# Optimization experiments

Measured on AMD Instinct MI355X. Metric: run time of the kernel, lower is better.

## Reference

```python
import jax, jax.numpy as jnp
import numpy as np

ATOM_FEA = 128
NBR_FEA = 64
NUM_NBR = 12
N_NODES = 50000
N_EDGES = N_NODES * NUM_NBR
BN_EPS = 1e-5


def setup_inputs() -> dict:
    key = jax.random.key(0)
    ks = jax.random.split(key, 8)
    x = jax.random.normal(ks[0], (N_NODES, ATOM_FEA), dtype=jnp.float32)
    # CGCNN layout: each node has exactly NUM_NBR edges, contiguous by source node
    src = jnp.repeat(jnp.arange(N_NODES, dtype=jnp.int64), NUM_NBR)
    nbr = jax.random.randint(ks[1], (N_EDGES,), 0, N_NODES, dtype=jnp.int64)
    edge_index = jnp.stack([src, nbr], axis=0)
    edge_attr = jax.random.normal(ks[2], (N_EDGES, NBR_FEA), dtype=jnp.float32)
    in_dim = 2 * ATOM_FEA + NBR_FEA
    out_dim = 2 * ATOM_FEA
    lim = 1.0 / np.sqrt(in_dim)
    W = jax.random.uniform(ks[3], (out_dim, in_dim), jnp.float32, -lim, lim)
    b = jax.random.uniform(ks[4], (out_dim,), jnp.float32, -lim, lim)
    bn1_g = jnp.ones((out_dim,), jnp.float32)
    bn1_b = jnp.zeros((out_dim,), jnp.float32)
    bn2_g = jnp.ones((ATOM_FEA,), jnp.float32)
    bn2_b = jnp.zeros((ATOM_FEA,), jnp.float32)
    return {"x": x, "edge_index": edge_index, "edge_attr": edge_attr,
            "W": W, "b": b, "bn1_g": bn1_g, "bn1_b": bn1_b,
            "bn2_g": bn2_g, "bn2_b": bn2_b}


def _batchnorm(h, gamma, beta):
    # training-mode BN: biased batch variance, eps=1e-5 (torch default)
    mean = jnp.mean(h, axis=0)
    var = jnp.var(h, axis=0)
    return (h - mean) * jax.lax.rsqrt(var + BN_EPS) * gamma + beta


def reference(x, edge_index, edge_attr, W, b, bn1_g, bn1_b, bn2_g, bn2_b):
    n_nodes, fea = x.shape
    num_nbr = edge_index.shape[1] // n_nodes
    # gather + concat: [E, 2F + nbr_fea]
    total = jnp.concatenate([x[edge_index[1]], x[edge_index[0]], edge_attr], axis=1)
    gated = total @ W.T + b                      # [E, 2F]
    gated = _batchnorm(gated, bn1_g, bn1_b)
    nbr_filter, nbr_core = jnp.split(gated, 2, axis=1)
    msg = jax.nn.sigmoid(nbr_filter) * jax.nn.softplus(nbr_core)  # [E, F]
    nbr_sumed = msg.reshape(n_nodes, num_nbr, fea).sum(axis=1)    # [N, F]
    nbr_sumed = _batchnorm(nbr_sumed, bn2_g, bn2_b)
    return jax.nn.softplus(x + nbr_sumed)
```

## Files before the change

kernel.cpp:

```cpp
#include <hip/hip_runtime.h>
#include <math.h>

#define ATOM_FEA 128
#define NBR_FEA  64
#define IN_DIM   320
#define OUT_DIM  256

#define M_TILE   48
#define GRID_G   1024

typedef float  f32x4 __attribute__((ext_vector_type(4)));
typedef short  s16x8 __attribute__((ext_vector_type(8)));

__device__ __forceinline__ float softplusf(float v) {
    float e = __expf(-fabsf(v));
    return fmaxf(v, 0.f) + __logf(1.f + e);
}
__device__ __forceinline__ float sigmoidf(float v) {
    return __builtin_amdgcn_rcpf(1.f + __expf(-v));
}
__device__ __forceinline__ unsigned short f2bf(float f) {
    unsigned u = __float_as_uint(f);
    return (unsigned short)((u + 0x7FFFu + ((u >> 16) & 1u)) >> 16);
}
__device__ __forceinline__ float bf2f(unsigned short h) {
    return __uint_as_float(((unsigned)h) << 16);
}
__device__ __forceinline__ unsigned pk2(float a, float b) {
    return (unsigned)f2bf(a) | ((unsigned)f2bf(b) << 16);
}

#define EA_OFF   0
#define EA_STR   144
#define X_OFF    6912
#define X_STR    520
#define SMEM2    31872

__global__ __launch_bounds__(256) void k1_nodegemm(
    const float* __restrict__ x, const float* __restrict__ W,
    float* __restrict__ A, float* __restrict__ B, int nNodes)
{
    __shared__ float sx[64][68];
    __shared__ float sw[64][68];
    const int tx = threadIdx.x & 15;
    const int ty = threadIdx.x >> 4;
    const int cTile = blockIdx.x * 64;
    const int nTile = blockIdx.y * 64;
    const int rBase = (cTile < 256) ? cTile : (cTile - 256);
    const int kBase = (cTile < 256) ? 0 : 128;

    float acc[4][4] = {};
    for (int kc = 0; kc < 2; ++kc) {
        int idx = threadIdx.x;
        #pragma unroll
        for (int i = 0; i < 4; ++i, idx += 256) {
            int n = idx >> 4, q = idx & 15;
            float4 v = make_float4(0.f, 0.f, 0.f, 0.f);
            int gn = nTile + n;
            if (gn < nNodes)
                v = *(const float4*)(x + (size_t)gn * ATOM_FEA + kc * 64 + q * 4);
            *(float4*)(&sx[n][q * 4]) = v;
        }
        idx = threadIdx.x;
        #pragma unroll
        for (int i = 0; i < 4; ++i, idx += 256) {
            int c = idx >> 4, q = idx & 15;
            float4 v = *(const float4*)(W + (size_t)(rBase + c) * IN_DIM + kBase + kc * 64 + q * 4);
            sw[q * 4 + 0][c] = v.x; sw[q * 4 + 1][c] = v.y;
            sw[q * 4 + 2][c] = v.z; sw[q * 4 + 3][c] = v.w;
        }
        __syncthreads();
        #pragma unroll
        for (int k = 0; k < 64; k += 2) {
            float4 w0 = *(const float4*)(&sw[k][tx * 4]);
            float4 w1 = *(const float4*)(&sw[k + 1][tx * 4]);
            float2 xv[4];
            #pragma unroll
            for (int i = 0; i < 4; ++i)
                xv[i] = *(const float2*)(&sx[ty * 4 + i][k]);
            #pragma unroll
            for (int i = 0; i < 4; ++i) {
                acc[i][0] = fmaf(xv[i].x, w0.x, fmaf(xv[i].y, w1.x, acc[i][0]));
                acc[i][1] = fmaf(xv[i].x, w0.y, fmaf(xv[i].y, w1.y, acc[i][1]));
                acc[i][2] = fmaf(xv[i].x, w0.z, fmaf(xv[i].y, w1.z, acc[i][2]));
                acc[i][3] = fmaf(xv[i].x, w0.w, fmaf(xv[i].y, w1.w, acc[i][3]));
            }
        }
        __syncthreads();
    }
    float* dst = (cTile < 256) ? A : B;
    const int cOff = (cTile < 256) ? cTile : (cTile - 256);
    #pragma unroll
    for (int i = 0; i < 4; ++i) {
        int gn = nTile + ty * 4 + i;
        if (gn < nNodes) {
            float4 v = make_float4(acc[i][0], acc[i][1], acc[i][2], acc[i][3]);
            *(float4*)(dst + (size_t)gn * 256 + cOff + tx * 4) = v;
        }
    }
}

__global__ __launch_bounds__(256) void k2_fused(
    const float* __restrict__ A, const float* __restrict__ Bm,
    const float* __restrict__ ea, const int* __restrict__ ei,
    const float* __restrict__ W, const float* __restrict__ bvec,
    unsigned short* __restrict__ gated, float* __restrict__ part,
    int nNodes, int nEdges)
{
    __shared__ alignas(16) char smem[SMEM2];
    const int tid  = threadIdx.x;
    const int wave = tid >> 6;
    const int lane = tid & 63;
    const int li   = lane & 15;
    const int quad = lane >> 4;

    s16x8 bfr[2][4];
    #pragma unroll
    for (int ks = 0; ks < 2; ++ks)
        #pragma unroll
        for (int ns = 0; ns < 4; ++ns) {
            int chn = wave * 64 + ns * 16 + li;
            const float* wr = W + (size_t)chn * IN_DIM + 256 + ks * 32 + quad * 8;
            float4 va = *(const float4*)wr;
            float4 vb = *(const float4*)(wr + 4);
            union { uint4 u; s16x8 v; } cv;
            cv.u = make_uint4(pk2(va.x, va.y), pk2(va.z, va.w),
                              pk2(vb.x, vb.y), pk2(vb.z, vb.w));
            bfr[ks][ns] = cv.v;
        }

    const int chq = lane;
    const float4 b4 = *(const float4*)(bvec + chq * 4);
    float4 s4  = {0.f, 0.f, 0.f, 0.f};
    float4 s24 = {0.f, 0.f, 0.f, 0.f};

    const int nTiles = (nEdges + M_TILE - 1) / M_TILE;
    for (int t = blockIdx.x; t < nTiles; t += gridDim.x) {
        const int tBase = t * M_TILE;
        #pragma unroll
        for (int i = 0; i < 3; ++i) {
            int idx = tid + i * 256;
            int r = idx >> 4, q = idx & 15;
            int ge = tBase + r;
            float4 v = make_float4(0.f, 0.f, 0.f, 0.f);
            if (ge < nEdges) v = *(const float4*)(ea + (size_t)ge * 64 + q * 4);
            uint2 u; u.x = pk2(v.x, v.y); u.y = pk2(v.z, v.w);
            *(uint2*)(smem + EA_OFF + r * EA_STR + q * 8) = u;
        }
        __syncthreads();

        s16x8 af[2][3];
        #pragma unroll
        for (int ks = 0; ks < 2; ++ks)
            #pragma unroll
            for (int ms = 0; ms < 3; ++ms)
                af[ks][ms] = *(const s16x8*)(smem + EA_OFF + (ms * 16 + li) * EA_STR + (ks * 32 + quad * 8) * 2);

        f32x4 acc[3][4] = {};
        #pragma unroll
        for (int ks = 0; ks < 2; ++ks)
            #pragma unroll
            for (int ms = 0; ms < 3; ++ms)
                #pragma unroll
                for (int ns = 0; ns < 4; ++ns)
                    acc[ms][ns] = __builtin_amdgcn_mfma_f32_16x16x32_bf16(
                        af[ks][ms], bfr[ks][ns], acc[ms][ns], 0, 0, 0);

        #pragma unroll
        for (int ms = 0; ms < 3; ++ms)
            #pragma unroll
            for (int ns = 0; ns < 4; ++ns) {
                int col = wave * 64 + ns * 16 + li;
                #pragma unroll
                for (int r = 0; r < 4; ++r) {
                    int row = ms * 16 + quad * 4 + r;
                    *(unsigned short*)(smem + X_OFF + row * X_STR + col * 2) = f2bf(acc[ms][ns][r]);
                }
            }
        __syncthreads();

        const int node = t * 4 + wave;
        if (node < nNodes) {
            const float4 Bn = *(const float4*)(Bm + (size_t)node * 256 + chq * 4);
            const int e0 = tBase + wave * 12;
            #pragma unroll
            for (int j = 0; j < 12; ++j) {
                const int e = e0 + j;
                const int nb = ei[nEdges + e];
                float4 a4 = *(const float4*)(A + (size_t)nb * 256 + chq * 4);
                uint2 xv = *(const uint2*)(smem + X_OFF + (wave * 12 + j) * X_STR + chq * 8);
                float g0 = bf2f((unsigned short)(xv.x & 0xffffu)) + a4.x + Bn.x + b4.x;
                float g1 = bf2f((unsigned short)(xv.x >> 16))     + a4.y + Bn.y + b4.y;
                float g2 = bf2f((unsigned short)(xv.y & 0xffffu)) + a4.z + Bn.z + b4.z;
                float g3 = bf2f((unsigned short)(xv.y >> 16))     + a4.w + Bn.w + b4.w;
                s4.x += g0; s4.y += g1; s4.z += g2; s4.w += g3;
                s24.x = fmaf(g0, g0, s24.x); s24.y = fmaf(g1, g1, s24.y);
                s24.z = fmaf(g2, g2, s24.z); s24.w = fmaf(g3, g3, s24.w);
                uint2 o; o.x = pk2(g0, g1); o.y = pk2(g2, g3);
                *(uint2*)(gated + (size_t)e * 256 + chq * 4) = o;
            }
        }
    }

    __syncthreads();
    float* red = (float*)smem;
    *(float4*)(red + (size_t)(wave * 64 + chq) * 8)     = s4;
    *(float4*)(red + (size_t)(wave * 64 + chq) * 8 + 4) = s24;
    __syncthreads();
    {
        const int c = tid;
        const int g = c >> 2, k = c & 3;
        float s = 0.f, s2 = 0.f;
        #pragma unroll
        for (int w = 0; w < 4; ++w) {
            s  += red[(w * 64 + g) * 8 + k];
            s2 += red[(w * 64 + g) * 8 + 4 + k];
        }
        part[(size_t)blockIdx.x * 512 + c]       = s;
        part[(size_t)blockIdx.x * 512 + 256 + c] = s2;
    }
}

__global__ __launch_bounds__(1024) void k2b_reduce(
    const float* __restrict__ part, const float* __restrict__ g1v,
    const float* __restrict__ b1v, float* __restrict__ stats,
    int nBlocks, float invE)
{
    __shared__ float4 red[8][128];
    const int cq = threadIdx.x & 127;
    const int g  = threadIdx.x >> 7;
    float4 s = {0.f, 0.f, 0.f, 0.f};
    for (int i = g; i < nBlocks; i += 8) {
        float4 v = *(const float4*)(part + (size_t)i * 512 + cq * 4);
        s.x += v.x; s.y += v.y; s.z += v.z; s.w += v.w;
    }
    red[g][cq] = s;
    __syncthreads();
    if (threadIdx.x < 256) {
        const int c = threadIdx.x;
        float sT = 0.f, s2T = 0.f;
        #pragma unroll
        for (int w = 0; w < 8; ++w) {
            const float* r = (const float*)&red[w][0];
            sT  += r[c];
            s2T += r[256 + c];
        }
        float mean = sT * invE;
        float var = fmaf(-mean, mean, s2T * invE);
        float sc = g1v[c] * rsqrtf(var + 1e-5f);
        stats[c] = sc;
        stats[256 + c] = fmaf(-mean, sc, b1v[c]);
    }
}

__global__ __launch_bounds__(256) void k3_msg2(
    const unsigned short* __restrict__ gated, const float* __restrict__ stats,
    float* __restrict__ NS, float* __restrict__ part2, int nNodes)
{
    const int tid = threadIdx.x;
    const int o  = tid & 15;
    const int nl = tid >> 4;
    float scF[8], shF[8], scC[8], shC[8];
    #pragma unroll
    for (int k = 0; k < 8; ++k) {
        int cf = o * 8 + k;
        scF[k] = stats[cf];        shF[k] = stats[256 + cf];
        scC[k] = stats[128 + cf];  shC[k] = stats[384 + cf];
    }
    float sA[8] = {}, s2A[8] = {};
    for (int n = blockIdx.x * 16 + nl; n < nNodes; n += gridDim.x * 16) {
        float m[8] = {};
        for (int j = 0; j < 12; ++j) {
            size_t base = (size_t)(n * 12 + j) * 256;
            uint4 uf = *(const uint4*)(gated + base + o * 8);
            uint4 uc = *(const uint4*)(gated + base + 128 + o * 8);
            unsigned fu[4] = {uf.x, uf.y, uf.z, uf.w};
            unsigned cu[4] = {uc.x, uc.y, uc.z, uc.w};
            #pragma unroll
            for (int q = 0; q < 4; ++q) {
                float f0 = fmaf(bf2f((unsigned short)(fu[q] & 0xffffu)), scF[q*2],   shF[q*2]);
                float f1 = fmaf(bf2f((unsigned short)(fu[q] >> 16)),     scF[q*2+1], shF[q*2+1]);
                float c0 = fmaf(bf2f((unsigned short)(cu[q] & 0xffffu)), scC[q*2],   shC[q*2]);
                float c1 = fmaf(bf2f((unsigned short)(cu[q] >> 16)),     scC[q*2+1], shC[q*2+1]);
                m[q*2]   = fmaf(sigmoidf(f0), softplusf(c0), m[q*2]);
                m[q*2+1] = fmaf(sigmoidf(f1), softplusf(c1), m[q*2+1]);
            }
        }
        float4 o0 = {m[0], m[1], m[2], m[3]};
        float4 o1 = {m[4], m[5], m[6], m[7]};
        *(float4*)(NS + (size_t)n * 128 + o * 8)     = o0;
        *(float4*)(NS + (size_t)n * 128 + o * 8 + 4) = o1;
        #pragma unroll
        for (int k = 0; k < 8; ++k) {
            sA[k] += m[k];
            s2A[k] = fmaf(m[k], m[k], s2A[k]);
        }
    }
    __shared__ float red[2][16][128];
    #pragma unroll
    for (int k = 0; k < 8; ++k) {
        red[0][nl][o * 8 + k] = sA[k];
        red[1][nl][o * 8 + k] = s2A[k];
    }
    __syncthreads();
    if (tid < 128) {
        float s = 0.f, s2 = 0.f;
        #pragma unroll
        for (int r = 0; r < 16; ++r) {
            s  += red[0][r][tid];
            s2 += red[1][r][tid];
        }
        part2[(size_t)blockIdx.x * 256 + tid]       = s;
        part2[(size_t)blockIdx.x * 256 + 128 + tid] = s2;
    }
}

__global__ __launch_bounds__(1024) void k3b_reduce(
    const float* __restrict__ part2, const float* __restrict__ g2v,
    const float* __restrict__ b2v, float* __restrict__ stats2,
    int nBlocks, float invN)
{
    __shared__ float4 red[16][64];
    const int cq = threadIdx.x & 63;
    const int g  = threadIdx.x >> 6;
    float4 s = {0.f, 0.f, 0.f, 0.f};
    for (int i = g; i < nBlocks; i += 16) {
        float4 v = *(const float4*)(part2 + (size_t)i * 256 + cq * 4);
        s.x += v.x; s.y += v.y; s.z += v.z; s.w += v.w;
    }
    red[g][cq] = s;
    __syncthreads();
    if (threadIdx.x < 128) {
        const int c = threadIdx.x;
        float sT = 0.f, s2T = 0.f;
        #pragma unroll
        for (int w = 0; w < 16; ++w) {
            const float* r = (const float*)&red[w][0];
            sT  += r[c];
            s2T += r[128 + c];
        }
        float mean = sT * invN;
        float var = fmaf(-mean, mean, s2T * invN);
        float sc = g2v[c] * rsqrtf(var + 1e-5f);
        stats2[c] = sc;
        stats2[128 + c] = fmaf(-mean, sc, b2v[c]);
    }
}

__global__ __launch_bounds__(256) void k4_final(
    const float* __restrict__ x, const float* __restrict__ ns,
    const float* __restrict__ stats2, float* __restrict__ out, int total4)
{
    int idx = blockIdx.x * 256 + threadIdx.x;
    for (int i = idx; i < total4; i += gridDim.x * 256) {
        int cq = i & 31;
        float4 xv = ((const float4*)x)[i];
        float4 sv = ((const float4*)ns)[i];
        float4 sc = ((const float4*)stats2)[cq];
        float4 sh = ((const float4*)(stats2 + 128))[cq];
        float4 o;
        o.x = softplusf(fmaf(sv.x, sc.x, sh.x) + xv.x);
        o.y = softplusf(fmaf(sv.y, sc.y, sh.y) + xv.y);
        o.z = softplusf(fmaf(sv.z, sc.z, sh.z) + xv.z);
        o.w = softplusf(fmaf(sv.w, sc.w, sh.w) + xv.w);
        ((float4*)out)[i] = o;
    }
}

extern "C" void kernel_launch(void* const* d_in, const int* in_sizes, int n_in,
                              void* d_out, int out_size, void* d_ws, size_t ws_size,
                              hipStream_t stream)
{
    const float* x   = (const float*)d_in[0];
    const int*   ei  = (const int*)d_in[1];
    const float* ea  = (const float*)d_in[2];
    const float* W   = (const float*)d_in[3];
    const float* b   = (const float*)d_in[4];
    const float* g1v = (const float*)d_in[5];
    const float* b1v = (const float*)d_in[6];
    const float* g2v = (const float*)d_in[7];
    const float* b2v = (const float*)d_in[8];
    float* out = (float*)d_out;

    const int nNodes = in_sizes[0] / ATOM_FEA;
    const int nEdges = in_sizes[1] / 2;

    float* ws = (float*)d_ws;
    float* A   = ws;
    float* Bm  = A   + (size_t)nNodes * 256;
    float* NS  = Bm  + (size_t)nNodes * 256;
    float* P1  = NS  + (size_t)nNodes * 128;
    float* P2  = P1  + (size_t)GRID_G * 512;
    float* S1  = P2  + (size_t)GRID_G * 256;
    float* S2  = S1  + 512;
    unsigned short* gated = (unsigned short*)(S2 + 256);
    (void)ws_size; (void)n_in; (void)out_size;

    dim3 grid1(8, (nNodes + 63) / 64);
    k1_nodegemm<<<grid1, 256, 0, stream>>>(x, W, A, Bm, nNodes);

    k2_fused<<<GRID_G, 256, 0, stream>>>(A, Bm, ea, ei, W, b, gated, P1, nNodes, nEdges);
    k2b_reduce<<<1, 1024, 0, stream>>>(P1, g1v, b1v, S1, GRID_G, 1.f / (float)nEdges);
    k3_msg2<<<GRID_G, 256, 0, stream>>>(gated, S1, NS, P2, nNodes);
    k3b_reduce<<<1, 1024, 0, stream>>>(P2, g2v, b2v, S2, GRID_G, 1.f / (float)nNodes);
    k4_final<<<2048, 256, 0, stream>>>(x, NS, S2, out, nNodes * 32);
}
```

Before: 675.3 us.

## Use MFMA bf16 node GEMM, bf16 A/B tables, two-stage stat reductions

```diff
diff --git a/kernel.cpp b/kernel.cpp
--- a/kernel.cpp
+++ b/kernel.cpp
@@ -7,7 +7,9 @@
 #define OUT_DIM  256
 
 #define M_TILE   48
-#define GRID_G   1024
+#define GRID_G   768
+#define GRID_3   1024
+#define RB1      32
 
 typedef float  f32x4 __attribute__((ext_vector_type(4)));
 typedef short  s16x8 __attribute__((ext_vector_type(8)));
@@ -36,72 +38,73 @@
 #define X_STR    520
 #define SMEM2    31872
 
-__global__ __launch_bounds__(256) void k1_nodegemm(
+__global__ __launch_bounds__(256) void k1_mfma(
     const float* __restrict__ x, const float* __restrict__ W,
-    float* __restrict__ A, float* __restrict__ B, int nNodes)
-{
-    __shared__ float sx[64][68];
-    __shared__ float sw[64][68];
-    const int tx = threadIdx.x & 15;
-    const int ty = threadIdx.x >> 4;
+    unsigned short* __restrict__ Abf, unsigned short* __restrict__ Bbf,
+    int nNodes)
+{
+    __shared__ alignas(16) char sx[64 * 272];
+    const int tid  = threadIdx.x;
+    const int wave = tid >> 6;
+    const int lane = tid & 63;
+    const int li   = lane & 15;
+    const int quad = lane >> 4;
     const int cTile = blockIdx.x * 64;
     const int nTile = blockIdx.y * 64;
-    const int rBase = (cTile < 256) ? cTile : (cTile - 256);
+    const int cOff  = (cTile < 256) ? cTile : (cTile - 256);
     const int kBase = (cTile < 256) ? 0 : 128;
-
-    float acc[4][4] = {};
-    for (int kc = 0; kc < 2; ++kc) {
-        int idx = threadIdx.x;
-        #pragma unroll
-        for (int i = 0; i < 4; ++i, idx += 256) {
-            int n = idx >> 4, q = idx & 15;
-            float4 v = make_float4(0.f, 0.f, 0.f, 0.f);
-            int gn = nTile + n;
-            if (gn < nNodes)
-                v = *(const float4*)(x + (size_t)gn * ATOM_FEA + kc * 64 + q * 4);
-            *(float4*)(&sx[n][q * 4]) = v;
-        }
-        idx = threadIdx.x;
-        #pragma unroll
-        for (int i = 0; i < 4; ++i, idx += 256) {
-            int c = idx >> 4, q = idx & 15;
-            float4 v = *(const float4*)(W + (size_t)(rBase + c) * IN_DIM + kBase + kc * 64 + q * 4);
-            sw[q * 4 + 0][c] = v.x; sw[q * 4 + 1][c] = v.y;
-            sw[q * 4 + 2][c] = v.z; sw[q * 4 + 3][c] = v.w;
-        }
-        __syncthreads();
-        #pragma unroll
-        for (int k = 0; k < 64; k += 2) {
-            float4 w0 = *(const float4*)(&sw[k][tx * 4]);
-            float4 w1 = *(const float4*)(&sw[k + 1][tx * 4]);
-            float2 xv[4];
-            #pragma unroll
-            for (int i = 0; i < 4; ++i)
-                xv[i] = *(const float2*)(&sx[ty * 4 + i][k]);
-            #pragma unroll
-            for (int i = 0; i < 4; ++i) {
-                acc[i][0] = fmaf(xv[i].x, w0.x, fmaf(xv[i].y, w1.x, acc[i][0]));
-                acc[i][1] = fmaf(xv[i].x, w0.y, fmaf(xv[i].y, w1.y, acc[i][1]));
-                acc[i][2] = fmaf(xv[i].x, w0.z, fmaf(xv[i].y, w1.z, acc[i][2]));
-                acc[i][3] = fmaf(xv[i].x, w0.w, fmaf(xv[i].y, w1.w, acc[i][3]));
-            }
-        }
-        __syncthreads();
-    }
-    float* dst = (cTile < 256) ? A : B;
-    const int cOff = (cTile < 256) ? cTile : (cTile - 256);
-    #pragma unroll
-    for (int i = 0; i < 4; ++i) {
-        int gn = nTile + ty * 4 + i;
-        if (gn < nNodes) {
-            float4 v = make_float4(acc[i][0], acc[i][1], acc[i][2], acc[i][3]);
-            *(float4*)(dst + (size_t)gn * 256 + cOff + tx * 4) = v;
-        }
-    }
+    unsigned short* dst = (cTile < 256) ? Abf : Bbf;
+
+    s16x8 bf[4][4];
+    #pragma unroll
+    for (int ks = 0; ks < 4; ++ks)
+        #pragma unroll
+        for (int ns = 0; ns < 4; ++ns) {
+            const float* wr = W + (size_t)(cOff + ns * 16 + li) * IN_DIM + kBase + ks * 32 + quad * 8;
+            float4 va = *(const float4*)wr;
+            float4 vb = *(const float4*)(wr + 4);
+            union { uint4 u; s16x8 v; } cv;
+            cv.u = make_uint4(pk2(va.x, va.y), pk2(va.z, va.w),
+                              pk2(vb.x, vb.y), pk2(vb.z, vb.w));
+            bf[ks][ns] = cv.v;
+        }
+
+    #pragma unroll
+    for (int i = 0; i < 8; ++i) {
+        int idx = tid + i * 256;
+        int r = idx >> 5, q = idx & 31;
+        int gn = nTile + r;
+        float4 v = make_float4(0.f, 0.f, 0.f, 0.f);
+        if (gn < nNodes) v = *(const float4*)(x + (size_t)gn * ATOM_FEA + q * 4);
+        uint2 u; u.x = pk2(v.x, v.y); u.y = pk2(v.z, v.w);
+        *(uint2*)(sx + r * 272 + q * 8) = u;
+    }
+    __syncthreads();
+
+    s16x8 af[4];
+    #pragma unroll
+    for (int ks = 0; ks < 4; ++ks)
+        af[ks] = *(const s16x8*)(sx + (wave * 16 + li) * 272 + (ks * 32 + quad * 8) * 2);
+
+    f32x4 acc[4] = {};
+    #pragma unroll
+    for (int ks = 0; ks < 4; ++ks)
+        #pragma unroll
+        for (int ns = 0; ns < 4; ++ns)
+            acc[ns] = __builtin_amdgcn_mfma_f32_16x16x32_bf16(af[ks], bf[ks][ns], acc[ns], 0, 0, 0);
+
+    #pragma unroll
+    for (int ns = 0; ns < 4; ++ns)
+        #pragma unroll
+        for (int r = 0; r < 4; ++r) {
+            int node = nTile + wave * 16 + quad * 4 + r;
+            if (node < nNodes)
+                dst[(size_t)node * 256 + cOff + ns * 16 + li] = f2bf(acc[ns][r]);
+        }
 }
 
 __global__ __launch_bounds__(256) void k2_fused(
-    const float* __restrict__ A, const float* __restrict__ Bm,
+    const unsigned short* __restrict__ Abf, const unsigned short* __restrict__ Bbf,
     const float* __restrict__ ea, const int* __restrict__ ei,
     const float* __restrict__ W, const float* __restrict__ bvec,
     unsigned short* __restrict__ gated, float* __restrict__ part,
@@ -181,18 +184,22 @@
 
         const int node = t * 4 + wave;
         if (node < nNodes) {
-            const float4 Bn = *(const float4*)(Bm + (size_t)node * 256 + chq * 4);
+            uint2 bn2 = *(const uint2*)(Bbf + (size_t)node * 256 + chq * 4);
+            const float Bn0 = bf2f((unsigned short)(bn2.x & 0xffffu));
+            const float Bn1 = bf2f((unsigned short)(bn2.x >> 16));
+            const float Bn2 = bf2f((unsigned short)(bn2.y & 0xffffu));
+            const float Bn3 = bf2f((unsigned short)(bn2.y >> 16));
             const int e0 = tBase + wave * 12;
             #pragma unroll
             for (int j = 0; j < 12; ++j) {
                 const int e = e0 + j;
                 const int nb = ei[nEdges + e];
-                float4 a4 = *(const float4*)(A + (size_t)nb * 256 + chq * 4);
+                uint2 a2 = *(const uint2*)(Abf + (size_t)nb * 256 + chq * 4);
                 uint2 xv = *(const uint2*)(smem + X_OFF + (wave * 12 + j) * X_STR + chq * 8);
-                float g0 = bf2f((unsigned short)(xv.x & 0xffffu)) + a4.x + Bn.x + b4.x;
-                float g1 = bf2f((unsigned short)(xv.x >> 16))     + a4.y + Bn.y + b4.y;
-                float g2 = bf2f((unsigned short)(xv.y & 0xffffu)) + a4.z + Bn.z + b4.z;
-                float g3 = bf2f((unsigned short)(xv.y >> 16))     + a4.w + Bn.w + b4.w;
+                float g0 = bf2f((unsigned short)(xv.x & 0xffffu)) + bf2f((unsigned short)(a2.x & 0xffffu)) + Bn0 + b4.x;
+                float g1 = bf2f((unsigned short)(xv.x >> 16))     + bf2f((unsigned short)(a2.x >> 16))     + Bn1 + b4.y;
+                float g2 = bf2f((unsigned short)(xv.y & 0xffffu)) + bf2f((unsigned short)(a2.y & 0xffffu)) + Bn2 + b4.z;
+                float g3 = bf2f((unsigned short)(xv.y >> 16))     + bf2f((unsigned short)(a2.y >> 16))     + Bn3 + b4.w;
                 s4.x += g0; s4.y += g1; s4.z += g2; s4.w += g3;
                 s24.x = fmaf(g0, g0, s24.x); s24.y = fmaf(g1, g1, s24.y);
                 s24.z = fmaf(g2, g2, s24.z); s24.w = fmaf(g3, g3, s24.w);
@@ -221,36 +228,31 @@
     }
 }
 
-__global__ __launch_bounds__(1024) void k2b_reduce(
-    const float* __restrict__ part, const float* __restrict__ g1v,
-    const float* __restrict__ b1v, float* __restrict__ stats,
-    int nBlocks, float invE)
-{
-    __shared__ float4 red[8][128];
-    const int cq = threadIdx.x & 127;
-    const int g  = threadIdx.x >> 7;
-    float4 s = {0.f, 0.f, 0.f, 0.f};
-    for (int i = g; i < nBlocks; i += 8) {
-        float4 v = *(const float4*)(part + (size_t)i * 512 + cq * 4);
-        s.x += v.x; s.y += v.y; s.z += v.z; s.w += v.w;
-    }
-    red[g][cq] = s;
-    __syncthreads();
-    if (threadIdx.x < 256) {
-        const int c = threadIdx.x;
-        float sT = 0.f, s2T = 0.f;
-        #pragma unroll
-        for (int w = 0; w < 8; ++w) {
-            const float* r = (const float*)&red[w][0];
-            sT  += r[c];
-            s2T += r[256 + c];
-        }
-        float mean = sT * invE;
-        float var = fmaf(-mean, mean, s2T * invE);
-        float sc = g1v[c] * rsqrtf(var + 1e-5f);
-        stats[c] = sc;
-        stats[256 + c] = fmaf(-mean, sc, b1v[c]);
-    }
+__global__ __launch_bounds__(512) void k2b1(
+    const float* __restrict__ part, float* __restrict__ out, int nRows, int rowsPerBlk)
+{
+    const int c = threadIdx.x;
+    int r0 = blockIdx.x * rowsPerBlk;
+    int r1 = min(r0 + rowsPerBlk, nRows);
+    float s = 0.f;
+    for (int r = r0; r < r1; ++r) s += part[(size_t)r * 512 + c];
+    out[(size_t)blockIdx.x * 512 + c] = s;
+}
+__global__ __launch_bounds__(256) void k2b2(
+    const float* __restrict__ p1, const float* __restrict__ g1v,
+    const float* __restrict__ b1v, float* __restrict__ stats, float invE)
+{
+    const int c = threadIdx.x;
+    float s = 0.f, s2 = 0.f;
+    for (int r = 0; r < RB1; ++r) {
+        s  += p1[(size_t)r * 512 + c];
+        s2 += p1[(size_t)r * 512 + 256 + c];
+    }
+    float mean = s * invE;
+    float var = fmaf(-mean, mean, s2 * invE);
+    float sc = g1v[c] * rsqrtf(var + 1e-5f);
+    stats[c] = sc;
+    stats[256 + c] = fmaf(-mean, sc, b1v[c]);
 }
 
 __global__ __launch_bounds__(256) void k3_msg2(
@@ -315,36 +317,31 @@
     }
 }
 
-__global__ __launch_bounds__(1024) void k3b_reduce(
-    const float* __restrict__ part2, const float* __restrict__ g2v,
-    const float* __restrict__ b2v, float* __restrict__ stats2,
-    int nBlocks, float invN)
-{
-    __shared__ float4 red[16][64];
-    const int cq = threadIdx.x & 63;
-    const int g  = threadIdx.x >> 6;
-    float4 s = {0.f, 0.f, 0.f, 0.f};
-    for (int i = g; i < nBlocks; i += 16) {
-        float4 v = *(const float4*)(part2 + (size_t)i * 256 + cq * 4);
-        s.x += v.x; s.y += v.y; s.z += v.z; s.w += v.w;
-    }
-    red[g][cq] = s;
-    __syncthreads();
-    if (threadIdx.x < 128) {
-        const int c = threadIdx.x;
-        float sT = 0.f, s2T = 0.f;
-        #pragma unroll
-        for (int w = 0; w < 16; ++w) {
-            const float* r = (const float*)&red[w][0];
-            sT  += r[c];
-            s2T += r[128 + c];
-        }
-        float mean = sT * invN;
-        float var = fmaf(-mean, mean, s2T * invN);
-        float sc = g2v[c] * rsqrtf(var + 1e-5f);
-        stats2[c] = sc;
-        stats2[128 + c] = fmaf(-mean, sc, b2v[c]);
-    }
+__global__ __launch_bounds__(256) void k3b1(
+    const float* __restrict__ part2, float* __restrict__ out, int nRows, int rowsPerBlk)
+{
+    const int c = threadIdx.x;
+    int r0 = blockIdx.x * rowsPerBlk;
+    int r1 = min(r0 + rowsPerBlk, nRows);
+    float s = 0.f;
+    for (int r = r0; r < r1; ++r) s += part2[(size_t)r * 256 + c];
+    out[(size_t)blockIdx.x * 256 + c] = s;
+}
+__global__ __launch_bounds__(128) void k3b2(
+    const float* __restrict__ p1, const float* __restrict__ g2v,
+    const float* __restrict__ b2v, float* __restrict__ stats2, float invN)
+{
+    const int c = threadIdx.x;
+    float s = 0.f, s2 = 0.f;
+    for (int r = 0; r < RB1; ++r) {
+        s  += p1[(size_t)r * 256 + c];
+        s2 += p1[(size_t)r * 256 + 128 + c];
+    }
+    float mean = s * invN;
+    float var = fmaf(-mean, mean, s2 * invN);
+    float sc = g2v[c] * rsqrtf(var + 1e-5f);
+    stats2[c] = sc;
+    stats2[128 + c] = fmaf(-mean, sc, b2v[c]);
 }
 
 __global__ __launch_bounds__(256) void k4_final(
@@ -385,23 +382,26 @@
     const int nNodes = in_sizes[0] / ATOM_FEA;
     const int nEdges = in_sizes[1] / 2;
 
-    float* ws = (float*)d_ws;
-    float* A   = ws;
-    float* Bm  = A   + (size_t)nNodes * 256;
-    float* NS  = Bm  + (size_t)nNodes * 256;
+    unsigned short* Abf   = (unsigned short*)d_ws;
+    unsigned short* Bbf   = Abf + (size_t)nNodes * 256;
+    unsigned short* gated = Bbf + (size_t)nNodes * 256;
+    float* NS  = (float*)(gated + (size_t)nEdges * 256);
     float* P1  = NS  + (size_t)nNodes * 128;
-    float* P2  = P1  + (size_t)GRID_G * 512;
-    float* S1  = P2  + (size_t)GRID_G * 256;
-    float* S2  = S1  + 512;
-    unsigned short* gated = (unsigned short*)(S2 + 256);
+    float* P1b = P1  + (size_t)GRID_G * 512;
+    float* P2  = P1b + (size_t)RB1 * 512;
+    float* P2b = P2  + (size_t)GRID_3 * 256;
+    float* S1  = P2b + (size_t)RB1 * 256;
+    float* S2  = S1 + 512;
     (void)ws_size; (void)n_in; (void)out_size;
 
     dim3 grid1(8, (nNodes + 63) / 64);
-    k1_nodegemm<<<grid1, 256, 0, stream>>>(x, W, A, Bm, nNodes);
-
-    k2_fused<<<GRID_G, 256, 0, stream>>>(A, Bm, ea, ei, W, b, gated, P1, nNodes, nEdges);
-    k2b_reduce<<<1, 1024, 0, stream>>>(P1, g1v, b1v, S1, GRID_G, 1.f / (float)nEdges);
-    k3_msg2<<<GRID_G, 256, 0, stream>>>(gated, S1, NS, P2, nNodes);
-    k3b_reduce<<<1, 1024, 0, stream>>>(P2, g2v, b2v, S2, GRID_G, 1.f / (float)nNodes);
+    k1_mfma<<<grid1, 256, 0, stream>>>(x, W, Abf, Bbf, nNodes);
+
+    k2_fused<<<GRID_G, 256, 0, stream>>>(Abf, Bbf, ea, ei, W, b, gated, P1, nNodes, nEdges);
+    k2b1<<<RB1, 512, 0, stream>>>(P1, P1b, GRID_G, (GRID_G + RB1 - 1) / RB1);
+    k2b2<<<1, 256, 0, stream>>>(P1b, g1v, b1v, S1, 1.f / (float)nEdges);
+    k3_msg2<<<GRID_3, 256, 0, stream>>>(gated, S1, NS, P2, nNodes);
+    k3b1<<<RB1, 256, 0, stream>>>(P2, P2b, GRID_3, (GRID_3 + RB1 - 1) / RB1);
+    k3b2<<<1, 128, 0, stream>>>(P2b, g2v, b2v, S2, 1.f / (float)nNodes);
     k4_final<<<2048, 256, 0, stream>>>(x, NS, S2, out, nNodes * 32);
 }
```

Result: faster. 656.2 us (-2.8%).
